# Performance work log

Hardware: AMD Instinct MI355X
Metric: run time of the kernel (lower is better)

Reference implementation:

```python
import jax, jax.numpy as jnp
import numpy as np

N_NODES = 10000
N_EDGES = 300000
NUM_HIDDEN = 256
NUM_IN = 512
NUM_HEADS = 4


def _lin(key, fin, fout):
    kw, kb = jax.random.split(key)
    w = jax.random.normal(kw, (fin, fout), dtype=jnp.float32) * (1.0 / np.sqrt(fin))
    b = jax.random.normal(kb, (fout,), dtype=jnp.float32) * 0.01
    return w, b


def setup_inputs() -> dict:
    key = jax.random.key(0)
    ks = jax.random.split(key, 12)
    h_V = jax.random.normal(ks[0], (N_NODES, NUM_HIDDEN), dtype=jnp.float32)
    h_E = jax.random.normal(ks[1], (N_EDGES, NUM_IN), dtype=jnp.float32)
    center_id = jnp.sort(jax.random.randint(ks[2], (N_EDGES,), 0, N_NODES, dtype=jnp.int32))
    batch_id = jax.random.randint(ks[3], (N_EDGES,), 0, 8, dtype=jnp.int32)
    # W_V: Linear(num_in, H) -> GELU -> Linear(H, H) -> GELU -> Linear(H, H)
    wv1_w, wv1_b = _lin(ks[4], NUM_IN, NUM_HIDDEN)
    wv2_w, wv2_b = _lin(ks[5], NUM_HIDDEN, NUM_HIDDEN)
    wv3_w, wv3_b = _lin(ks[6], NUM_HIDDEN, NUM_HIDDEN)
    # Bias: Linear(3H, H) -> ReLU -> Linear(H, H) -> ReLU -> Linear(H, num_heads)
    b1_w, b1_b = _lin(ks[7], 3 * NUM_HIDDEN, NUM_HIDDEN)
    b2_w, b2_b = _lin(ks[8], NUM_HIDDEN, NUM_HIDDEN)
    b3_w, b3_b = _lin(ks[9], NUM_HIDDEN, NUM_HEADS)
    # W_O: Linear(H, H, bias=False)
    wo_w, _ = _lin(ks[10], NUM_HIDDEN, NUM_HIDDEN)
    return {
        "h_V": h_V, "h_E": h_E,
        "wv1_w": wv1_w, "wv1_b": wv1_b, "wv2_w": wv2_w, "wv2_b": wv2_b,
        "wv3_w": wv3_w, "wv3_b": wv3_b,
        "b1_w": b1_w, "b1_b": b1_b, "b2_w": b2_w, "b2_b": b2_b,
        "b3_w": b3_w, "b3_b": b3_b,
        "wo_w": wo_w,
        "center_id": center_id, "batch_id": batch_id,
    }


def reference(h_V, h_E, wv1_w, wv1_b, wv2_w, wv2_b, wv3_w, wv3_b,
              b1_w, b1_b, b2_w, b2_b, b3_w, b3_b, wo_w,
              center_id, batch_id):
    N = h_V.shape[0]
    E = h_E.shape[0]
    n_heads = NUM_HEADS
    d = h_V.shape[1] // n_heads  # head dim

    # Bias MLP on gathered center node feats concat edge feats -> per-edge, per-head logit
    x = jnp.concatenate([h_V[center_id], h_E], axis=-1)  # [E, 3H]
    x = jax.nn.relu(x @ b1_w + b1_b)
    x = jax.nn.relu(x @ b2_w + b2_b)
    w = x @ b3_w + b3_b                                   # [E, n_heads]
    logits = w / np.float32(np.sqrt(d))

    # W_V MLP (exact GELU, matching torch nn.GELU default)
    v = jax.nn.gelu(h_E @ wv1_w + wv1_b, approximate=False)
    v = jax.nn.gelu(v @ wv2_w + wv2_b, approximate=False)
    v = (v @ wv3_w + wv3_b).reshape(E, n_heads, d)        # [E, n_heads, d]

    # scatter_softmax over edges sharing the same center node
    seg_max = jax.ops.segment_max(logits, center_id, num_segments=N)  # [N, n_heads]
    p = jnp.exp(logits - seg_max[center_id])                          # [E, n_heads]
    denom = jax.ops.segment_sum(p, center_id, num_segments=N)         # [N, n_heads]
    attend = p / denom[center_id]                                     # [E, n_heads]

    # weighted scatter-sum of values
    out = jax.ops.segment_sum(attend[:, :, None] * v, center_id, num_segments=N)
    out = out.reshape(N, n_heads * d)                                 # [N, H]
    return out @ wo_w
```

## Files before the change

kernel.cpp:

```cpp
#include <hip/hip_runtime.h>
#include <hip/hip_bf16.h>
#include <math.h>

#define H 256
#define NIN 512
#define NHEADS 4
#define BM 64
#define LOG2E 1.4426950408889634f

typedef __attribute__((ext_vector_type(8))) short short8;
typedef __attribute__((ext_vector_type(4))) short short4v;
typedef __attribute__((ext_vector_type(4))) float floatx4;

__device__ __forceinline__ float4 ld4(const float* p){ return *reinterpret_cast<const float4*>(p); }

__device__ __forceinline__ short f2bf(float x){
    __hip_bfloat16 h = __float2bfloat16(x);
    return *reinterpret_cast<short*>(&h);
}
__device__ __forceinline__ float bf2f(short h){
    return __uint_as_float(((unsigned)(unsigned short)h) << 16);
}
__device__ __forceinline__ float fexp2(float x){ return __builtin_amdgcn_exp2f(x); }
__device__ __forceinline__ float frcp(float x){ return __builtin_amdgcn_rcpf(x); }

__device__ __forceinline__ float gelu_fast(float x){
    float y = x * fmaf(x*x, 0.0356774081f, 0.7978845608f);
    float t = fexp2(-2.8853900818f * fabsf(y));
    float th = (1.f - t) * frcp(1.f + t);
    th = copysignf(th, y);
    return 0.5f * x * (1.f + th);
}
__device__ __forceinline__ floatx4 mfma16(short8 a, short8 b, floatx4 c){
    return __builtin_amdgcn_mfma_f32_16x16x32_bf16(a, b, c, 0, 0, 0);
}
__device__ __forceinline__ short8 pack8(float4 a, float4 b){
    short8 v;
    v[0]=f2bf(a.x); v[1]=f2bf(a.y); v[2]=f2bf(a.z); v[3]=f2bf(a.w);
    v[4]=f2bf(b.x); v[5]=f2bf(b.y); v[6]=f2bf(b.z); v[7]=f2bf(b.w);
    return v;
}

#define ZERO_ACC() do { \
    _Pragma("unroll") \
    for (int i_=0;i_<4;i_++){ \
        _Pragma("unroll") \
        for (int j_=0;j_<4;j_++) acc[i_][j_] = (floatx4){0.f,0.f,0.f,0.f}; \
    } \
} while(0)

#define LOADB(DST, WF, NCH, CH) do { \
    _Pragma("unroll") \
    for (int s_=0;s_<2;s_++) \
        _Pragma("unroll") \
        for (int n_=0;n_<4;n_++) \
            DST[s_][n_] = *reinterpret_cast<const short8*>( \
                &(WF)[(size_t)((((w*4+n_)*(NCH) + (CH))*2 + s_) << 9) + lane*8]); \
} while(0)

#define COPYB(DST, SRC) do { \
    _Pragma("unroll") \
    for (int s_=0;s_<2;s_++) \
        _Pragma("unroll") \
        for (int n_=0;n_<4;n_++) DST[s_][n_] = SRC[s_][n_]; \
} while(0)

#define MFMA_LDS(BC, ABASE, ASTR) do { \
    _Pragma("unroll") \
    for (int s_=0;s_<2;s_++){ \
        short8 af_[4]; \
        _Pragma("unroll") \
        for (int rb_=0;rb_<4;rb_++) \
            af_[rb_] = *reinterpret_cast<const short8*>( \
                &(ABASE)[(rb_*16+lr)*(ASTR) + s_*32 + lh*8]); \
        _Pragma("unroll") \
        for (int n_=0;n_<4;n_++) \
            _Pragma("unroll") \
            for (int rb_=0;rb_<4;rb_++) \
                acc[rb_][n_] = mfma16(af_[rb_], BC[s_][n_], acc[rb_][n_]); \
    } \
} while(0)

#define MFMA_GLB(BC, CH) do { \
    _Pragma("unroll") \
    for (int s_=0;s_<2;s_++){ \
        short8 af_[4]; \
        _Pragma("unroll") \
        for (int rb_=0;rb_<4;rb_++) \
            af_[rb_] = *reinterpret_cast<const short8*>( \
                arow[rb_] + (CH)*64 + s_*32 + lh*8); \
        _Pragma("unroll") \
        for (int n_=0;n_<4;n_++) \
            _Pragma("unroll") \
            for (int rb_=0;rb_<4;rb_++) \
                acc[rb_][n_] = mfma16(af_[rb_], BC[s_][n_], acc[rb_][n_]); \
    } \
} while(0)

__global__ void k_ranges(const int* __restrict__ center, int* __restrict__ start, int E, int N)
{
    int n = blockIdx.x*blockDim.x + threadIdx.x;
    if (n > N) return;
    if (n == N){ start[N] = E; return; }
    int lo = 0, hi = E;
    while (lo < hi){ int mid = (lo+hi)>>1; if (center[mid] < n) lo = mid+1; else hi = mid; }
    start[n] = lo;
}

__global__ void __launch_bounds__(256)
k_wconvf(const float* __restrict__ src, short* __restrict__ dst, int KK)
{
    const int cb = blockIdx.x;
    const int ch = blockIdx.y;
    const int NCH = KK >> 6;
    const int t = threadIdx.x;
    const int s = t >> 7;
    const int rem = t & 127;
    const int ln = rem >> 1;
    const int j0 = (rem & 1) * 4;
    const int k = ch*64 + s*32 + ((ln>>4)<<3) + j0;
    const int col = cb*16 + (ln & 15);
    short4v o;
    o[0] = f2bf(src[(size_t)(k+0)*H + col]);
    o[1] = f2bf(src[(size_t)(k+1)*H + col]);
    o[2] = f2bf(src[(size_t)(k+2)*H + col]);
    o[3] = f2bf(src[(size_t)(k+3)*H + col]);
    *reinterpret_cast<short4v*>(&dst[(size_t)(((cb*NCH + ch)*2 + s) << 9) + ln*8 + j0]) = o;
}

__global__ void k_w3padf(const float* __restrict__ b3w, short* __restrict__ dst)
{
    const int t = threadIdx.x;
    const int ch = t >> 6, ln = t & 63;
    const int col = ln & 15;
    #pragma unroll
    for (int s=0;s<2;s++){
        #pragma unroll
        for (int j=0;j<8;j++){
            int k = ch*64 + s*32 + ((ln>>4)<<3) + j;
            dst[((ch*2 + s) << 9) + ln*8 + j] =
                (col < NHEADS) ? f2bf(b3w[(size_t)k*NHEADS + col]) : (short)0;
        }
    }
}

__global__ void __launch_bounds__(256)
k_nodebias(const float* __restrict__ hV, const float* __restrict__ b1w,
           const float* __restrict__ b1b, float* __restrict__ nb, int N)
{
    __shared__ float ps[8][260];
    const int n0 = blockIdx.x*8;
    const int tid = threadIdx.x;
    {
        int r = tid >> 5, cq = (tid & 31)*8;
        *reinterpret_cast<float4*>(&ps[r][cq])   = ld4(&hV[(size_t)(n0+r)*H + cq]);
        *reinterpret_cast<float4*>(&ps[r][cq+4]) = ld4(&hV[(size_t)(n0+r)*H + cq + 4]);
    }
    __syncthreads();
    float a[8];
    float bias = b1b[tid];
    #pragma unroll
    for (int i=0;i<8;i++) a[i] = bias;
    #pragma unroll 4
    for (int k=0;k<H;k++){
        float w = b1w[(size_t)k*H + tid];
        #pragma unroll
        for (int i=0;i<8;i++) a[i] = fmaf(ps[i][k], w, a[i]);
    }
    #pragma unroll
    for (int i=0;i<8;i++) nb[(size_t)(n0+i)*H + tid] = a[i];
}

__global__ void __launch_bounds__(256,3)
k_bias2(const float* __restrict__ hE,
        const short* __restrict__ Wf1,
        const short* __restrict__ Wf2,
        const short* __restrict__ W3f,
        const float* __restrict__ b3b,
        const float* __restrict__ b2b,
        const float* __restrict__ nodebias,
        const int* __restrict__ center,
        float* __restrict__ logits,
        short* __restrict__ hEb, int E)
{
    __shared__ short Alds[2][BM][72];
    __shared__ short xarena[BM][264];
    __shared__ int   csh[BM];

    const int tid = threadIdx.x;
    const int lane = tid & 63, w = tid >> 6;
    const int lr = lane & 15, lh = lane >> 4;
    const int e0 = blockIdx.x * BM;
    const int srow = tid >> 2, skq = tid & 3;
    const int gsrow = (e0 + srow < E) ? (e0 + srow) : (E-1);
    const float* aSrc = hE + (size_t)gsrow * NIN + skq * 16;
    short* ebDst = hEb + (size_t)gsrow * NIN + skq * 16;

    if (tid < BM){ int ge = e0 + tid; csh[tid] = center[ge < E ? ge : E-1]; }

    floatx4 acc[4][4];
    ZERO_ACC();

    short8 bc[2][4], bn[2][4];
    LOADB(bc, Wf1, 8, 0);
    float4 pf[4];
    #pragma unroll
    for (int q=0;q<4;q++) pf[q] = ld4(aSrc + q*4);
    {
        short8 s8a = pack8(pf[0], pf[1]), s8b = pack8(pf[2], pf[3]);
        *reinterpret_cast<short8*>(&Alds[0][srow][skq*16])   = s8a;
        *reinterpret_cast<short8*>(&Alds[0][srow][skq*16+8]) = s8b;
        *reinterpret_cast<short8*>(ebDst)     = s8a;
        *reinterpret_cast<short8*>(ebDst + 8) = s8b;
    }
    __syncthreads();

    #pragma unroll
    for (int ch = 0; ch < 8; ch++){
        if (ch < 7){
            LOADB(bn, Wf1, 8, ch+1);
            #pragma unroll
            for (int q=0;q<4;q++) pf[q] = ld4(aSrc + (ch+1)*64 + q*4);
        }
        __builtin_amdgcn_s_setprio(1);
        MFMA_LDS(bc, &Alds[ch&1][0][0], 72);
        __builtin_amdgcn_s_setprio(0);
        if (ch < 7){
            short8 s8a = pack8(pf[0], pf[1]), s8b = pack8(pf[2], pf[3]);
            *reinterpret_cast<short8*>(&Alds[(ch&1)^1][srow][skq*16])   = s8a;
            *reinterpret_cast<short8*>(&Alds[(ch&1)^1][srow][skq*16+8]) = s8b;
            *reinterpret_cast<short8*>(ebDst + (ch+1)*64)     = s8a;
            *reinterpret_cast<short8*>(ebDst + (ch+1)*64 + 8) = s8b;
            COPYB(bc, bn);
        }
        __syncthreads();
    }
    const int c0 = w * 64;
    #pragma unroll
    for (int rb=0;rb<4;rb++)
        #pragma unroll
        for (int j=0;j<4;j++){
            const int row = rb*16 + lh*4 + j;
            const float* nb = nodebias + (size_t)csh[row]*H + c0 + lr;
            #pragma unroll
            for (int n=0;n<4;n++)
                xarena[row][c0 + n*16 + lr] = f2bf(fmaxf(acc[rb][n][j] + nb[n*16], 0.f));
        }
    __syncthreads();

    ZERO_ACC();
    LOADB(bc, Wf2, 4, 0);
    #pragma unroll
    for (int ch = 0; ch < 4; ch++){
        if (ch < 3) LOADB(bn, Wf2, 4, ch+1);
        __builtin_amdgcn_s_setprio(1);
        MFMA_LDS(bc, &xarena[0][ch*64], 264);
        __builtin_amdgcn_s_setprio(0);
        if (ch < 3) COPYB(bc, bn);
    }
    float bb[4];
    #pragma unroll
    for (int n=0;n<4;n++) bb[n] = b2b[c0 + n*16 + lr];
    __syncthreads();
    #pragma unroll
    for (int rb=0;rb<4;rb++)
        #pragma unroll
        for (int j=0;j<4;j++){
            const int row = rb*16 + lh*4 + j;
            #pragma unroll
            for (int n=0;n<4;n++)
                xarena[row][c0 + n*16 + lr] = f2bf(fmaxf(acc[rb][n][j] + bb[n], 0.f));
        }
    __syncthreads();

    floatx4 a3 = (floatx4){0.f,0.f,0.f,0.f};
    #pragma unroll
    for (int ch=0;ch<4;ch++)
        #pragma unroll
        for (int s=0;s<2;s++){
            short8 bfr = *reinterpret_cast<const short8*>(&W3f[((ch*2+s)<<9) + lane*8]);
            short8 af = *reinterpret_cast<const short8*>(&xarena[w*16+lr][ch*64 + s*32 + lh*8]);
            a3 = mfma16(af, bfr, a3);
        }
    if (lr < NHEADS){
        float bias = b3b[lr];
        #pragma unroll
        for (int j=0;j<4;j++){
            int ge = e0 + w*16 + lh*4 + j;
            if (ge < E) logits[(size_t)ge*NHEADS + lr] = (a3[j] + bias) * 0.125f;
        }
    }
}

__global__ void k_smstats(const float* __restrict__ logits, const int* __restrict__ start,
                          float* __restrict__ mbuf, float* __restrict__ dbuf)
{
    int n = blockIdx.x;
    int s = start[n], e_end = start[n+1];
    int lane = threadIdx.x;
    int i = lane >> 2, hh = lane & 3;
    float mx = -INFINITY;
    for (int b = s + i; b < e_end; b += 16) mx = fmaxf(mx, logits[(size_t)b*NHEADS + hh]);
    #pragma unroll
    for (int off=4; off<64; off<<=1) mx = fmaxf(mx, __shfl_xor(mx, off, 64));
    float sum = 0.f;
    for (int b = s + i; b < e_end; b += 16) sum += expf(logits[(size_t)b*NHEADS + hh] - mx);
    #pragma unroll
    for (int off=4; off<64; off<<=1) sum += __shfl_xor(sum, off, 64);
    if (lane < 4){ mbuf[(size_t)n*NHEADS + hh] = mx; dbuf[(size_t)n*NHEADS + hh] = sum; }
}

__global__ void __launch_bounds__(256,3)
k_wv2(const short* __restrict__ hEb,
      const short* __restrict__ Wf1, const float* __restrict__ b1v,
      const short* __restrict__ Wf2, const float* __restrict__ b2v,
      const short* __restrict__ Wf3, const float* __restrict__ b3v,
      const int* __restrict__ center, const float* __restrict__ logits,
      const float* __restrict__ mbuf, const float* __restrict__ dbuf,
      float* __restrict__ pre, int E)
{
    __shared__ short xarena[BM][264];
    __shared__ int   csh[BM];

    const int tid = threadIdx.x;
    const int lane = tid & 63, w = tid >> 6;
    const int lr = lane & 15, lh = lane >> 4;
    const int e0 = blockIdx.x * BM;

    if (tid < BM){ int ge = e0 + tid; csh[tid] = center[ge < E ? ge : E-1]; }

    const short* arow[4];
    #pragma unroll
    for (int rb=0;rb<4;rb++){
        int r = e0 + rb*16 + lr; if (r >= E) r = E-1;
        arow[rb] = hEb + (size_t)r*NIN;
    }

    floatx4 acc[4][4];
    ZERO_ACC();

    short8 bc[2][4], bn[2][4];
    LOADB(bc, Wf1, 8, 0);

    #pragma unroll
    for (int ch = 0; ch < 8; ch++){
        if (ch < 7) LOADB(bn, Wf1, 8, ch+1);
        __builtin_amdgcn_s_setprio(1);
        MFMA_GLB(bc, ch);
        __builtin_amdgcn_s_setprio(0);
        if (ch < 7) COPYB(bc, bn);
    }
    const int c0 = w * 64;
    __syncthreads();
    {
        float bcv[4];
        #pragma unroll
        for (int n=0;n<4;n++) bcv[n] = b1v[c0 + n*16 + lr];
        #pragma unroll
        for (int rb=0;rb<4;rb++)
            #pragma unroll
            for (int j=0;j<4;j++){
                const int row = rb*16 + lh*4 + j;
                #pragma unroll
                for (int n=0;n<4;n++)
                    xarena[row][c0 + n*16 + lr] = f2bf(gelu_fast(acc[rb][n][j] + bcv[n]));
            }
    }
    __syncthreads();

    ZERO_ACC();
    LOADB(bc, Wf2, 4, 0);
    #pragma unroll
    for (int ch = 0; ch < 4; ch++){
        if (ch < 3) LOADB(bn, Wf2, 4, ch+1);
        __builtin_amdgcn_s_setprio(1);
        MFMA_LDS(bc, &xarena[0][ch*64], 264);
        __builtin_amdgcn_s_setprio(0);
        if (ch < 3) COPYB(bc, bn);
    }
    float bc2[4];
    #pragma unroll
    for (int n=0;n<4;n++) bc2[n] = b2v[c0 + n*16 + lr];
    __syncthreads();
    #pragma unroll
    for (int rb=0;rb<4;rb++)
        #pragma unroll
        for (int j=0;j<4;j++){
            const int row = rb*16 + lh*4 + j;
            #pragma unroll
            for (int n=0;n<4;n++)
                xarena[row][c0 + n*16 + lr] = f2bf(gelu_fast(acc[rb][n][j] + bc2[n]));
        }
    __syncthreads();

    ZERO_ACC();
    LOADB(bc, Wf3, 4, 0);
    #pragma unroll
    for (int ch = 0; ch < 4; ch++){
        if (ch < 3) LOADB(bn, Wf3, 4, ch+1);
        __builtin_amdgcn_s_setprio(1);
        MFMA_LDS(bc, &xarena[0][ch*64], 264);
        __builtin_amdgcn_s_setprio(0);
        if (ch < 3) COPYB(bc, bn);
    }
    float bc3[4];
    #pragma unroll
    for (int n=0;n<4;n++) bc3[n] = b3v[c0 + n*16 + lr];
    __syncthreads();

    #pragma unroll
    for (int rb=0;rb<4;rb++)
        #pragma unroll
        for (int j=0;j<4;j++){
            const int row = rb*16 + lh*4 + j;
            const int ge = e0 + row;
            float att = 0.f;
            if (ge < E){
                const int c = csh[row];
                att = fexp2((logits[(size_t)ge*NHEADS + w] - mbuf[(size_t)c*NHEADS + w]) * LOG2E)
                      * frcp(dbuf[(size_t)c*NHEADS + w]);
            }
            #pragma unroll
            for (int n=0;n<4;n++)
                xarena[row][c0 + n*16 + lr] = f2bf((acc[rb][n][j] + bc3[n]) * att);
        }
    __syncthreads();
    {
        const int col = tid;
        float s = 0.f; int cur = csh[0];
        for (int e=0;e<BM;e++){
            int c = csh[e];
            if (c != cur){ atomicAdd(&pre[(size_t)cur*H + col], s); s = 0.f; cur = c; }
            s += bf2f(xarena[e][col]);
        }
        atomicAdd(&pre[(size_t)cur*H + col], s);
    }
}

__global__ void __launch_bounds__(256)
k_out(const float* __restrict__ pre, const float* __restrict__ wo,
      float* __restrict__ out, int N)
{
    __shared__ float ps[8][260];
    const int tid = threadIdx.x;
    const int nb = blockIdx.x * 8;
    {
        int r = tid >> 5, c = (tid & 31) * 8;
        *reinterpret_cast<float4*>(&ps[r][c])   = ld4(&pre[(size_t)(nb+r)*H + c]);
        *reinterpret_cast<float4*>(&ps[r][c+4]) = ld4(&pre[(size_t)(nb+r)*H + c+4]);
    }
    __syncthreads();
    float a[8];
    #pragma unroll
    for (int i=0;i<8;i++) a[i]=0.f;
    #pragma unroll 4
    for (int k=0;k<H;k++){
        float w = wo[(size_t)k*H + tid];
        #pragma unroll
        for (int i=0;i<8;i++) a[i] = fmaf(ps[i][k], w, a[i]);
    }
    #pragma unroll
    for (int i=0;i<8;i++)
        out[(size_t)(nb+i)*H + tid] = a[i];
}

extern "C" void kernel_launch(void* const* d_in, const int* in_sizes, int n_in,
                              void* d_out, int out_size, void* d_ws, size_t ws_size,
                              hipStream_t stream)
{
    const float* hV   = (const float*)d_in[0];
    const float* hE   = (const float*)d_in[1];
    const float* wv1w = (const float*)d_in[2];
    const float* wv1b = (const float*)d_in[3];
    const float* wv2w = (const float*)d_in[4];
    const float* wv2b = (const float*)d_in[5];
    const float* wv3w = (const float*)d_in[6];
    const float* wv3b = (const float*)d_in[7];
    const float* b1w  = (const float*)d_in[8];
    const float* b1b  = (const float*)d_in[9];
    const float* b2w  = (const float*)d_in[10];
    const float* b2b  = (const float*)d_in[11];
    const float* b3w  = (const float*)d_in[12];
    const float* b3b  = (const float*)d_in[13];
    const float* wow  = (const float*)d_in[14];
    const int*   center = (const int*)d_in[15];

    const int E = in_sizes[15];
    const int N = in_sizes[0] / H;
    const int nblk = (E + BM - 1) / BM;

    float* pre      = (float*)d_ws;
    float* logits   = pre + (size_t)N*H;
    float* mbuf     = logits + (size_t)E*NHEADS;
    float* dbuf     = mbuf + (size_t)N*NHEADS;
    int*   start    = (int*)(dbuf + (size_t)N*NHEADS);
    float* nodebias = (float*)(start + ((N+1+3)&~3));
    short* wf1b     = (short*)(nodebias + (size_t)N*H);
    short* wf2b     = wf1b + 512*256;
    short* w3fb     = wf2b + 256*256;
    short* wf1v     = w3fb + 16*256;
    short* wf2v     = wf1v + 512*256;
    short* wf3v     = wf2v + 256*256;
    short* hEb      = wf3v + 256*256;

    hipMemsetAsync(pre, 0, (size_t)N*H*sizeof(float), stream);
    k_ranges<<<(N+1+255)/256, 256, 0, stream>>>(center, start, E, N);
    k_wconvf<<<dim3(16,8), 256, 0, stream>>>(b1w + 256*H, wf1b, 512);
    k_wconvf<<<dim3(16,4), 256, 0, stream>>>(b2w,  wf2b, 256);
    k_w3padf<<<1, 256, 0, stream>>>(b3w, w3fb);
    k_wconvf<<<dim3(16,8), 256, 0, stream>>>(wv1w, wf1v, 512);
    k_wconvf<<<dim3(16,4), 256, 0, stream>>>(wv2w, wf2v, 256);
    k_wconvf<<<dim3(16,4), 256, 0, stream>>>(wv3w, wf3v, 256);
    k_nodebias<<<N/8, 256, 0, stream>>>(hV, b1w, b1b, nodebias, N);
    k_bias2<<<nblk, 256, 0, stream>>>(hE, wf1b, wf2b, w3fb, b3b, b2b, nodebias, center,
                                      logits, hEb, E);
    k_smstats<<<N, 64, 0, stream>>>(logits, start, mbuf, dbuf);
    k_wv2<<<nblk, 256, 0, stream>>>(hEb, wf1v, wv1b, wf2v, wv2b, wf3v, wv3b,
                                    center, logits, mbuf, dbuf, pre, E);
    k_out<<<N/8, 256, 0, stream>>>(pre, wow, (float*)d_out, N);
}
```

Baseline: 771.7 us.

## Convert hE to swizzled bf16 upfront and stage A tiles via async LDS loads

A separate conversion kernel now writes hE to bf16 with an XOR-swizzled column layout, and k_bias2 no longer converts fp32 inputs itself. Both k_bias2 and k_wv2 stage A-operand chunks into a 4-deep LDS ring using global_load_lds, with manual vmcnt waits and barriers, and read fragments through the swizzle to avoid bank conflicts. This replaces direct global fragment loads in k_wv2 and register-staged conversion in k_bias2 with asynchronous copies that overlap the MFMA work. The risks are an extra launch and pass over hE, hand-tuned vmcnt counts that must match the exact number of issued loads, and reads past E in the last block since the staged rows are no longer clamped.

```diff
diff --git a/kernel.cpp b/kernel.cpp
--- a/kernel.cpp
+++ b/kernel.cpp
@@ -40,6 +40,13 @@
     v[4]=f2bf(b.x); v[5]=f2bf(b.y); v[6]=f2bf(b.z); v[7]=f2bf(b.w);
     return v;
 }
+__device__ __forceinline__ void gload16(const short* g, short* l){
+    __builtin_amdgcn_global_load_lds(
+        (const __attribute__((address_space(1))) unsigned int*)(const void*)g,
+        (__attribute__((address_space(3))) unsigned int*)(void*)l, 16, 0, 0);
+}
+
+#define VMCNT(N) asm volatile("s_waitcnt vmcnt(" #N ")" ::: "memory")
 
 #define ZERO_ACC() do { \
     _Pragma("unroll") \
@@ -81,14 +88,15 @@
     } \
 } while(0)
 
-#define MFMA_GLB(BC, CH) do { \
+#define MFMA_SWZ(BC, CH) do { \
+    const short* sb_ = smem + (((CH)&3)<<12); \
     _Pragma("unroll") \
     for (int s_=0;s_<2;s_++){ \
         short8 af_[4]; \
         _Pragma("unroll") \
         for (int rb_=0;rb_<4;rb_++) \
             af_[rb_] = *reinterpret_cast<const short8*>( \
-                arow[rb_] + (CH)*64 + s_*32 + lh*8); \
+                &sb_[(rb_*16+lr)*64 + (((s_*4+lh) ^ (lr&7))<<3)]); \
         _Pragma("unroll") \
         for (int n_=0;n_<4;n_++) \
             _Pragma("unroll") \
@@ -97,6 +105,11 @@
     } \
 } while(0)
 
+#define STAGE(CH) do { \
+    gload16(gsrc0 + (CH)*64, smem + (((CH)&3)<<12) + (w*2+0)*512); \
+    gload16(gsrc1 + (CH)*64, smem + (((CH)&3)<<12) + (w*2+1)*512); \
+} while(0)
+
 __global__ void k_ranges(const int* __restrict__ center, int* __restrict__ start, int E, int N)
 {
     int n = blockIdx.x*blockDim.x + threadIdx.x;
@@ -105,6 +118,18 @@
     int lo = 0, hi = E;
     while (lo < hi){ int mid = (lo+hi)>>1; if (center[mid] < n) lo = mid+1; else hi = mid; }
     start[n] = lo;
+}
+
+__global__ void __launch_bounds__(256)
+k_conv(const float* __restrict__ hE, short* __restrict__ hEb)
+{
+    size_t idx = ((size_t)blockIdx.x*256 + threadIdx.x) * 8;
+    int r = (int)(idx >> 9);
+    int within = (int)(idx & 511);
+    int sl = (within >> 3) & 7;
+    int base = within & ~63;
+    float4 a = ld4(&hE[idx]), b = ld4(&hE[idx+4]);
+    *reinterpret_cast<short8*>(&hEb[(size_t)r*NIN + base + ((sl ^ (r&7))<<3)]) = pack8(a,b);
 }
 
 __global__ void __launch_bounds__(256)
@@ -172,7 +197,7 @@
 }
 
 __global__ void __launch_bounds__(256,3)
-k_bias2(const float* __restrict__ hE,
+k_bias2(const short* __restrict__ hEb,
         const short* __restrict__ Wf1,
         const short* __restrict__ Wf2,
         const short* __restrict__ W3f,
@@ -180,61 +205,47 @@
         const float* __restrict__ b2b,
         const float* __restrict__ nodebias,
         const int* __restrict__ center,
-        float* __restrict__ logits,
-        short* __restrict__ hEb, int E)
-{
-    __shared__ short Alds[2][BM][72];
-    __shared__ short xarena[BM][264];
+        float* __restrict__ logits, int E)
+{
+    __shared__ short smem[BM*264];
     __shared__ int   csh[BM];
 
     const int tid = threadIdx.x;
     const int lane = tid & 63, w = tid >> 6;
     const int lr = lane & 15, lh = lane >> 4;
     const int e0 = blockIdx.x * BM;
-    const int srow = tid >> 2, skq = tid & 3;
-    const int gsrow = (e0 + srow < E) ? (e0 + srow) : (E-1);
-    const float* aSrc = hE + (size_t)gsrow * NIN + skq * 16;
-    short* ebDst = hEb + (size_t)gsrow * NIN + skq * 16;
 
     if (tid < BM){ int ge = e0 + tid; csh[tid] = center[ge < E ? ge : E-1]; }
+
+    const short* gsrc0 = hEb + (size_t)(e0 + (w*2+0)*8 + (lane>>3))*NIN + (lane&7)*8;
+    const short* gsrc1 = hEb + (size_t)(e0 + (w*2+1)*8 + (lane>>3))*NIN + (lane&7)*8;
 
     floatx4 acc[4][4];
     ZERO_ACC();
 
     short8 bc[2][4], bn[2][4];
     LOADB(bc, Wf1, 8, 0);
-    float4 pf[4];
-    #pragma unroll
-    for (int q=0;q<4;q++) pf[q] = ld4(aSrc + q*4);
-    {
-        short8 s8a = pack8(pf[0], pf[1]), s8b = pack8(pf[2], pf[3]);
-        *reinterpret_cast<short8*>(&Alds[0][srow][skq*16])   = s8a;
-        *reinterpret_cast<short8*>(&Alds[0][srow][skq*16+8]) = s8b;
-        *reinterpret_cast<short8*>(ebDst)     = s8a;
-        *reinterpret_cast<short8*>(ebDst + 8) = s8b;
-    }
-    __syncthreads();
+    STAGE(0); STAGE(1);
 
     #pragma unroll
     for (int ch = 0; ch < 8; ch++){
-        if (ch < 7){
-            LOADB(bn, Wf1, 8, ch+1);
-            #pragma unroll
-            for (int q=0;q<4;q++) pf[q] = ld4(aSrc + (ch+1)*64 + q*4);
-        }
+        if (ch < 7) LOADB(bn, Wf1, 8, ch+1);
+        if (ch < 6) STAGE(ch+2);
+        if      (ch==0) VMCNT(4);
+        else if (ch==1) VMCNT(12);
+        else if (ch==6) VMCNT(18);
+        else if (ch==7) VMCNT(8);
+        else            VMCNT(20);
+        __builtin_amdgcn_s_barrier();
+        __builtin_amdgcn_sched_barrier(0);
         __builtin_amdgcn_s_setprio(1);
-        MFMA_LDS(bc, &Alds[ch&1][0][0], 72);
+        MFMA_SWZ(bc, ch);
         __builtin_amdgcn_s_setprio(0);
-        if (ch < 7){
-            short8 s8a = pack8(pf[0], pf[1]), s8b = pack8(pf[2], pf[3]);
-            *reinterpret_cast<short8*>(&Alds[(ch&1)^1][srow][skq*16])   = s8a;
-            *reinterpret_cast<short8*>(&Alds[(ch&1)^1][srow][skq*16+8]) = s8b;
-            *reinterpret_cast<short8*>(ebDst + (ch+1)*64)     = s8a;
-            *reinterpret_cast<short8*>(ebDst + (ch+1)*64 + 8) = s8b;
-            COPYB(bc, bn);
-        }
-        __syncthreads();
-    }
+        if (ch < 7) COPYB(bc, bn);
+    }
+    __syncthreads();
+
+    short (*xarena)[264] = reinterpret_cast<short(*)[264]>(smem);
     const int c0 = w * 64;
     #pragma unroll
     for (int rb=0;rb<4;rb++)
@@ -319,7 +330,7 @@
       const float* __restrict__ mbuf, const float* __restrict__ dbuf,
       float* __restrict__ pre, int E)
 {
-    __shared__ short xarena[BM][264];
+    __shared__ short smem[BM*264];
     __shared__ int   csh[BM];
 
     const int tid = threadIdx.x;
@@ -329,29 +340,36 @@
 
     if (tid < BM){ int ge = e0 + tid; csh[tid] = center[ge < E ? ge : E-1]; }
 
-    const short* arow[4];
-    #pragma unroll
-    for (int rb=0;rb<4;rb++){
-        int r = e0 + rb*16 + lr; if (r >= E) r = E-1;
-        arow[rb] = hEb + (size_t)r*NIN;
-    }
+    const short* gsrc0 = hEb + (size_t)(e0 + (w*2+0)*8 + (lane>>3))*NIN + (lane&7)*8;
+    const short* gsrc1 = hEb + (size_t)(e0 + (w*2+1)*8 + (lane>>3))*NIN + (lane&7)*8;
 
     floatx4 acc[4][4];
     ZERO_ACC();
 
     short8 bc[2][4], bn[2][4];
     LOADB(bc, Wf1, 8, 0);
+    STAGE(0); STAGE(1);
 
     #pragma unroll
     for (int ch = 0; ch < 8; ch++){
         if (ch < 7) LOADB(bn, Wf1, 8, ch+1);
+        if (ch < 6) STAGE(ch+2);
+        if      (ch==0) VMCNT(4);
+        else if (ch==1) VMCNT(12);
+        else if (ch==6) VMCNT(18);
+        else if (ch==7) VMCNT(8);
+        else            VMCNT(20);
+        __builtin_amdgcn_s_barrier();
+        __builtin_amdgcn_sched_barrier(0);
         __builtin_amdgcn_s_setprio(1);
-        MFMA_GLB(bc, ch);
+        MFMA_SWZ(bc, ch);
         __builtin_amdgcn_s_setprio(0);
         if (ch < 7) COPYB(bc, bn);
     }
+    __syncthreads();
+
+    short (*xarena)[264] = reinterpret_cast<short(*)[264]>(smem);
     const int c0 = w * 64;
-    __syncthreads();
     {
         float bcv[4];
         #pragma unroll
@@ -488,6 +506,7 @@
     const int E = in_sizes[15];
     const int N = in_sizes[0] / H;
     const int nblk = (E + BM - 1) / BM;
+    const int Epad = nblk * BM;
 
     float* pre      = (float*)d_ws;
     float* logits   = pre + (size_t)N*H;
@@ -511,9 +530,10 @@
     k_wconvf<<<dim3(16,8), 256, 0, stream>>>(wv1w, wf1v, 512);
     k_wconvf<<<dim3(16,4), 256, 0, stream>>>(wv2w, wf2v, 256);
     k_wconvf<<<dim3(16,4), 256, 0, stream>>>(wv3w, wf3v, 256);
+    k_conv<<<(int)(((size_t)E*NIN/8 + 255)/256), 256, 0, stream>>>(hE, hEb);
     k_nodebias<<<N/8, 256, 0, stream>>>(hV, b1w, b1b, nodebias, N);
-    k_bias2<<<nblk, 256, 0, stream>>>(hE, wf1b, wf2b, w3fb, b3b, b2b, nodebias, center,
-                                      logits, hEb, E);
+    k_bias2<<<nblk, 256, 0, stream>>>(hEb, wf1b, wf2b, w3fb, b3b, b2b, nodebias, center,
+                                      logits, E);
     k_smstats<<<N, 64, 0, stream>>>(logits, start, mbuf, dbuf);
     k_wv2<<<nblk, 256, 0, stream>>>(hEb, wf1v, wv1b, wf2v, wv2b, wf3v, wv3b,
                                     center, logits, mbuf, dbuf, pre, E);
```

Measured after the change: 687.5 us. 1.12x faster.

## Stage swizzled bf16 edge tiles into LDS via async global_load_lds in value kernel

Applied to the files above, without the earlier changes.

The bias kernel now writes the bf16 copy of h_E in an XOR-swizzled 8-element layout, and skips writes for out-of-range rows. The value-MLP kernel previously read A fragments straight from global memory. It now streams them with async global_load_lds into a 4-deep LDS ring, waits with explicit vmcnt counts, and reads with a matching swizzle to avoid bank conflicts. Barriers are replaced with an lgkmcnt wait plus s_barrier, so outstanding vector-memory loads are no longer drained at each sync. The hand-tuned vmcnt values and the shared layout contract between the two kernels are fragile. The tail block also reads beyond E, because the row clamp was removed from the staged loads.

```diff
diff --git a/kernel.cpp b/kernel.cpp
--- a/kernel.cpp
+++ b/kernel.cpp
@@ -40,6 +40,19 @@
     v[4]=f2bf(b.x); v[5]=f2bf(b.y); v[6]=f2bf(b.z); v[7]=f2bf(b.w);
     return v;
 }
+__device__ __forceinline__ void gload16(const short* g, short* l){
+    __builtin_amdgcn_global_load_lds(
+        (const __attribute__((address_space(1))) unsigned int*)(const void*)g,
+        (__attribute__((address_space(3))) unsigned int*)(void*)l, 16, 0, 0);
+}
+
+#define VMCNT(N) asm volatile("s_waitcnt vmcnt(" #N ")" ::: "memory")
+
+#define LGKM_BARRIER() do { \
+    asm volatile("s_waitcnt lgkmcnt(0)" ::: "memory"); \
+    __builtin_amdgcn_s_barrier(); \
+    __builtin_amdgcn_sched_barrier(0); \
+} while(0)
 
 #define ZERO_ACC() do { \
     _Pragma("unroll") \
@@ -81,20 +94,26 @@
     } \
 } while(0)
 
-#define MFMA_GLB(BC, CH) do { \
+#define MFMA_SWZ(BC, CH) do { \
+    const short* sb_ = smem + (((CH)&3)<<12); \
     _Pragma("unroll") \
     for (int s_=0;s_<2;s_++){ \
         short8 af_[4]; \
         _Pragma("unroll") \
         for (int rb_=0;rb_<4;rb_++) \
             af_[rb_] = *reinterpret_cast<const short8*>( \
-                arow[rb_] + (CH)*64 + s_*32 + lh*8); \
+                &sb_[(rb_*16+lr)*64 + (((s_*4+lh) ^ (lr&7))<<3)]); \
         _Pragma("unroll") \
         for (int n_=0;n_<4;n_++) \
             _Pragma("unroll") \
             for (int rb_=0;rb_<4;rb_++) \
                 acc[rb_][n_] = mfma16(af_[rb_], BC[s_][n_], acc[rb_][n_]); \
     } \
+} while(0)
+
+#define STAGE(CH) do { \
+    gload16(gsrc0 + (CH)*64, smem + (((CH)&3)<<12) + (w*2+0)*512); \
+    gload16(gsrc1 + (CH)*64, smem + (((CH)&3)<<12) + (w*2+1)*512); \
 } while(0)
 
 __global__ void k_ranges(const int* __restrict__ center, int* __restrict__ start, int E, int N)
@@ -192,9 +211,12 @@
     const int lr = lane & 15, lh = lane >> 4;
     const int e0 = blockIdx.x * BM;
     const int srow = tid >> 2, skq = tid & 3;
-    const int gsrow = (e0 + srow < E) ? (e0 + srow) : (E-1);
+    const bool rowOK = (e0 + srow) < E;
+    const int gsrow = rowOK ? (e0 + srow) : (E-1);
     const float* aSrc = hE + (size_t)gsrow * NIN + skq * 16;
-    short* ebDst = hEb + (size_t)gsrow * NIN + skq * 16;
+    short* ebBase = hEb + (size_t)gsrow * NIN;
+    const int sl0 = (2*skq)     ^ (srow & 7);
+    const int sl1 = (2*skq + 1) ^ (srow & 7);
 
     if (tid < BM){ int ge = e0 + tid; csh[tid] = center[ge < E ? ge : E-1]; }
 
@@ -210,10 +232,12 @@
         short8 s8a = pack8(pf[0], pf[1]), s8b = pack8(pf[2], pf[3]);
         *reinterpret_cast<short8*>(&Alds[0][srow][skq*16])   = s8a;
         *reinterpret_cast<short8*>(&Alds[0][srow][skq*16+8]) = s8b;
-        *reinterpret_cast<short8*>(ebDst)     = s8a;
-        *reinterpret_cast<short8*>(ebDst + 8) = s8b;
-    }
-    __syncthreads();
+        if (rowOK){
+            *reinterpret_cast<short8*>(ebBase + (sl0<<3)) = s8a;
+            *reinterpret_cast<short8*>(ebBase + (sl1<<3)) = s8b;
+        }
+    }
+    LGKM_BARRIER();
 
     #pragma unroll
     for (int ch = 0; ch < 8; ch++){
@@ -229,11 +253,13 @@
             short8 s8a = pack8(pf[0], pf[1]), s8b = pack8(pf[2], pf[3]);
             *reinterpret_cast<short8*>(&Alds[(ch&1)^1][srow][skq*16])   = s8a;
             *reinterpret_cast<short8*>(&Alds[(ch&1)^1][srow][skq*16+8]) = s8b;
-            *reinterpret_cast<short8*>(ebDst + (ch+1)*64)     = s8a;
-            *reinterpret_cast<short8*>(ebDst + (ch+1)*64 + 8) = s8b;
+            if (rowOK){
+                *reinterpret_cast<short8*>(ebBase + (ch+1)*64 + (sl0<<3)) = s8a;
+                *reinterpret_cast<short8*>(ebBase + (ch+1)*64 + (sl1<<3)) = s8b;
+            }
             COPYB(bc, bn);
         }
-        __syncthreads();
+        LGKM_BARRIER();
     }
     const int c0 = w * 64;
     #pragma unroll
@@ -246,7 +272,7 @@
             for (int n=0;n<4;n++)
                 xarena[row][c0 + n*16 + lr] = f2bf(fmaxf(acc[rb][n][j] + nb[n*16], 0.f));
         }
-    __syncthreads();
+    LGKM_BARRIER();
 
     ZERO_ACC();
     LOADB(bc, Wf2, 4, 0);
@@ -261,7 +287,7 @@
     float bb[4];
     #pragma unroll
     for (int n=0;n<4;n++) bb[n] = b2b[c0 + n*16 + lr];
-    __syncthreads();
+    LGKM_BARRIER();
     #pragma unroll
     for (int rb=0;rb<4;rb++)
         #pragma unroll
@@ -271,7 +297,7 @@
             for (int n=0;n<4;n++)
                 xarena[row][c0 + n*16 + lr] = f2bf(fmaxf(acc[rb][n][j] + bb[n], 0.f));
         }
-    __syncthreads();
+    LGKM_BARRIER();
 
     floatx4 a3 = (floatx4){0.f,0.f,0.f,0.f};
     #pragma unroll
@@ -319,7 +345,7 @@
       const float* __restrict__ mbuf, const float* __restrict__ dbuf,
       float* __restrict__ pre, int E)
 {
-    __shared__ short xarena[BM][264];
+    __shared__ short smem[BM*264];
     __shared__ int   csh[BM];
 
     const int tid = threadIdx.x;
@@ -329,29 +355,36 @@
 
     if (tid < BM){ int ge = e0 + tid; csh[tid] = center[ge < E ? ge : E-1]; }
 
-    const short* arow[4];
-    #pragma unroll
-    for (int rb=0;rb<4;rb++){
-        int r = e0 + rb*16 + lr; if (r >= E) r = E-1;
-        arow[rb] = hEb + (size_t)r*NIN;
-    }
+    const short* gsrc0 = hEb + (size_t)(e0 + (w*2+0)*8 + (lane>>3))*NIN + (lane&7)*8;
+    const short* gsrc1 = hEb + (size_t)(e0 + (w*2+1)*8 + (lane>>3))*NIN + (lane&7)*8;
 
     floatx4 acc[4][4];
     ZERO_ACC();
 
     short8 bc[2][4], bn[2][4];
     LOADB(bc, Wf1, 8, 0);
+    STAGE(0); STAGE(1);
 
     #pragma unroll
     for (int ch = 0; ch < 8; ch++){
         if (ch < 7) LOADB(bn, Wf1, 8, ch+1);
+        if (ch < 6) STAGE(ch+2);
+        if      (ch==0) VMCNT(4);
+        else if (ch==1) VMCNT(12);
+        else if (ch==6) VMCNT(18);
+        else if (ch==7) VMCNT(8);
+        else            VMCNT(20);
+        __builtin_amdgcn_s_barrier();
+        __builtin_amdgcn_sched_barrier(0);
         __builtin_amdgcn_s_setprio(1);
-        MFMA_GLB(bc, ch);
+        MFMA_SWZ(bc, ch);
         __builtin_amdgcn_s_setprio(0);
         if (ch < 7) COPYB(bc, bn);
     }
+    LGKM_BARRIER();
+
+    short (*xarena)[264] = reinterpret_cast<short(*)[264]>(smem);
     const int c0 = w * 64;
-    __syncthreads();
     {
         float bcv[4];
         #pragma unroll
@@ -366,7 +399,7 @@
                     xarena[row][c0 + n*16 + lr] = f2bf(gelu_fast(acc[rb][n][j] + bcv[n]));
             }
     }
-    __syncthreads();
+    LGKM_BARRIER();
 
     ZERO_ACC();
     LOADB(bc, Wf2, 4, 0);
@@ -381,7 +414,7 @@
     float bc2[4];
     #pragma unroll
     for (int n=0;n<4;n++) bc2[n] = b2v[c0 + n*16 + lr];
-    __syncthreads();
+    LGKM_BARRIER();
     #pragma unroll
     for (int rb=0;rb<4;rb++)
         #pragma unroll
@@ -391,7 +424,7 @@
             for (int n=0;n<4;n++)
                 xarena[row][c0 + n*16 + lr] = f2bf(gelu_fast(acc[rb][n][j] + bc2[n]));
         }
-    __syncthreads();
+    LGKM_BARRIER();
 
     ZERO_ACC();
     LOADB(bc, Wf3, 4, 0);
@@ -406,7 +439,7 @@
     float bc3[4];
     #pragma unroll
     for (int n=0;n<4;n++) bc3[n] = b3v[c0 + n*16 + lr];
-    __syncthreads();
+    LGKM_BARRIER();
 
     #pragma unroll
     for (int rb=0;rb<4;rb++)
@@ -424,7 +457,7 @@
             for (int n=0;n<4;n++)
                 xarena[row][c0 + n*16 + lr] = f2bf((acc[rb][n][j] + bc3[n]) * att);
         }
-    __syncthreads();
+    LGKM_BARRIER();
     {
         const int col = tid;
         float s = 0.f; int cur = csh[0];
```

After: 837.7 us. 8.6% more time.
